# Performance work log

Measured on AMD Instinct MI355X. Metric: run time of the kernel, lower is better.

## Reference

```python
import jax, jax.numpy as jnp
import numpy as np


def pairwise_distances(x):
    # squared euclidean distances, clamped at 0 (as in the torch source)
    sq = jnp.sum(x * x, axis=1)  # [N]
    dist = sq[:, None] + sq[None, :] - 2.0 * (x @ x.T)  # [N, N]
    return jnp.maximum(dist, 0.0)


def setup_inputs() -> dict:
    key = jax.random.key(0)
    k1, k2 = jax.random.split(key)
    N, D, T = 8192, 128, 1_000_000
    features = jax.random.normal(k1, (N, D), dtype=jnp.float32)
    triplets = jax.random.randint(k2, (T, 3), 0, N, dtype=jnp.int64)
    return {"features": features, "triplets": triplets}


def reference(features, triplets):
    dist = pairwise_distances(features)  # [N, N]
    i, j, k = triplets[:, 0], triplets[:, 1], triplets[:, 2]
    d_ij = dist[i, j]  # [T] gather
    d_ik = dist[i, k]  # [T] gather
    # log(1 + exp(d_ij - d_ik)) per triplet, mean over triplets
    per_triplet = jnp.logaddexp(0.0, d_ij - d_ik)
    loss = jnp.mean(per_triplet)
    return loss.reshape(1)  # torch returns FloatTensor([loss])
```

## Files before the change

kernel.cpp:

```cpp
#include <hip/hip_runtime.h>
#include <hip/hip_fp16.h>
#include <math.h>

constexpr int D = 128;
constexpr int MAIN_BLOCKS = 2048;
constexpr int BLOCK = 256;
constexpr int NWAVES = MAIN_BLOCKS * (BLOCK / 64);
constexpr int NROWS = 8192;

#define QSCALE 25.4f
#define TWO_S2 (2.0f * (5.0f / 127.0f) * (5.0f / 127.0f))

#if __has_builtin(__builtin_amdgcn_sdot4)
__device__ inline int dot4(unsigned a, unsigned b, int c) {
    return __builtin_amdgcn_sdot4(a, b, c, false);
}
#else
__device__ inline int dot4(unsigned a, unsigned b, int c) {
    c += (int)(char)(a) * (int)(char)(b);
    c += (int)(char)(a >> 8) * (int)(char)(b >> 8);
    c += (int)(char)(a >> 16) * (int)(char)(b >> 16);
    c += (int)(char)(a >> 24) * (int)(char)(b >> 24);
    return c;
}
#endif

__global__ __launch_bounds__(256) void prep_kernel(const float* __restrict__ feat,
                                                   const unsigned long long* __restrict__ trip,
                                                   int n_slots,
                                                   __half* __restrict__ sqh,
                                                   unsigned* __restrict__ q8,
                                                   int* __restrict__ flag, int N) {
    if (blockIdx.x == gridDim.x - 1) {
        if (threadIdx.x < 64) {
            int cnt = n_slots < 2048 ? n_slots : 2048;
            bool big = false;
            for (int idx = threadIdx.x; idx < cnt; idx += 64)
                big |= (trip[idx] >> 32) != 0ULL;
            unsigned long long b = __ballot(big);
            if (threadIdx.x == 0) flag[0] = (b != 0ULL) ? 1 : 0;
        }
        return;
    }
    int gidx = blockIdx.x * 256 + threadIdx.x;
    int row = gidx >> 5, lane = gidx & 31;
    if (row >= N) return;
    float4 v = ((const float4*)(feat + (size_t)row * D))[lane];
    float s = v.x * v.x + v.y * v.y + v.z * v.z + v.w * v.w;
#pragma unroll
    for (int m = 16; m >= 1; m >>= 1) s += __shfl_xor(s, m);
    if (lane == 0) sqh[row] = __float2half(s);
    int q0 = __float2int_rn(fminf(fmaxf(v.x * QSCALE, -127.f), 127.f));
    int q1 = __float2int_rn(fminf(fmaxf(v.y * QSCALE, -127.f), 127.f));
    int q2 = __float2int_rn(fminf(fmaxf(v.z * QSCALE, -127.f), 127.f));
    int q3 = __float2int_rn(fminf(fmaxf(v.w * QSCALE, -127.f), 127.f));
    unsigned p = (q0 & 255) | ((q1 & 255) << 8) | ((q2 & 255) << 16) | ((q3 & 255) << 24);
    q8[(size_t)row * 32 + lane] = p;
}

__global__ __launch_bounds__(256, 8) void triplet_kernel(const uint4* __restrict__ q8,
                                                         const void* __restrict__ trip_raw,
                                                         const __half* __restrict__ sqh,
                                                         const int* __restrict__ flag,
                                                         double* __restrict__ partial,
                                                         int T, int N) {
    __shared__ uint4 sq_u4[NROWS * 2 / 16];
    {
        const uint4* src = (const uint4*)sqh;
        int nvec = N * 2 / 16;
        for (int t = threadIdx.x; t < nvec; t += BLOCK) sq_u4[t] = src[t];
    }
    __syncthreads();
    const __half* sqs = (const __half*)sq_u4;

    const int lane = threadIdx.x & 63;
    const int sub = lane & 3;
    const int g = lane >> 2;
    const int wave = blockIdx.x * (BLOCK / 64) + (threadIdx.x >> 6);
    const int stride = gridDim.x * (BLOCK / 64) * 16;
    const bool m32 = (flag[0] != 0);
    const int* __restrict__ t32 = (const int*)trip_raw;
    const long long* __restrict__ t64 = (const long long*)trip_raw;

    double lsum = 0.0;
    for (int tb = wave * 16; tb < T; tb += stride) {
        int t = tb + g;
        bool valid = t < T;
        int tc = valid ? t : T - 1;
        int i, j, k;
        if (m32) { i = t32[3 * tc]; j = t32[3 * tc + 1]; k = t32[3 * tc + 2]; }
        else     { i = (int)t64[3 * tc]; j = (int)t64[3 * tc + 1]; k = (int)t64[3 * tc + 2]; }

        const uint4* pi = q8 + (size_t)i * 8 + sub;
        const uint4* pj = q8 + (size_t)j * 8 + sub;
        const uint4* pk = q8 + (size_t)k * 8 + sub;
        uint4 A0 = pi[0], A1 = pi[4];
        uint4 B0 = pj[0], B1 = pj[4];
        uint4 C0 = pk[0], C1 = pk[4];

        int d1 = 0, d2 = 0;
        d1 = dot4(A0.x, B0.x, d1); d1 = dot4(A0.y, B0.y, d1);
        d1 = dot4(A0.z, B0.z, d1); d1 = dot4(A0.w, B0.w, d1);
        d1 = dot4(A1.x, B1.x, d1); d1 = dot4(A1.y, B1.y, d1);
        d1 = dot4(A1.z, B1.z, d1); d1 = dot4(A1.w, B1.w, d1);
        d2 = dot4(A0.x, C0.x, d2); d2 = dot4(A0.y, C0.y, d2);
        d2 = dot4(A0.z, C0.z, d2); d2 = dot4(A0.w, C0.w, d2);
        d2 = dot4(A1.x, C1.x, d2); d2 = dot4(A1.y, C1.y, d2);
        d2 = dot4(A1.z, C1.z, d2); d2 = dot4(A1.w, C1.w, d2);

        int dd = d1 - d2;
        dd += __shfl_xor(dd, 1);
        dd += __shfl_xor(dd, 2);

        float sqj = __half2float(sqs[j]);
        float sqk = __half2float(sqs[k]);
        float z = (sqj - sqk) - TWO_S2 * (float)dd;
        float loss = fmaxf(z, 0.0f) + __logf(1.0f + __expf(-fabsf(z)));
        lsum += valid ? (double)loss : 0.0;
    }
#pragma unroll
    for (int m = 1; m < 64; m <<= 1) lsum += __shfl_xor(lsum, m);
    if (lane == 0) partial[wave] = lsum;
}

__global__ __launch_bounds__(256) void finalize_kernel(const double* __restrict__ partial,
                                                       int nw, float* __restrict__ out,
                                                       int T) {
    __shared__ double sm[256];
    double s = 0.0;
    for (int i = threadIdx.x; i < nw; i += blockDim.x) s += partial[i];
    sm[threadIdx.x] = s;
    __syncthreads();
    for (int w = 128; w >= 1; w >>= 1) {
        if ((int)threadIdx.x < w) sm[threadIdx.x] += sm[threadIdx.x + w];
        __syncthreads();
    }
    if (threadIdx.x == 0) out[0] = (float)(sm[0] / (4.0 * (double)T));
}

extern "C" void kernel_launch(void* const* d_in, const int* in_sizes, int n_in,
                              void* d_out, int out_size, void* d_ws, size_t ws_size,
                              hipStream_t stream) {
    const float* feat = (const float*)d_in[0];
    const void* trip = d_in[1];
    int N = in_sizes[0] / D;
    int T = in_sizes[1] / 3;

    char* ws = (char*)d_ws;
    int* flag = (int*)ws;
    double* partial = (double*)(ws + 256);
    __half* sqh = (__half*)(ws + 256 + 8 * (size_t)NWAVES);
    size_t q8_off = (256 + 8 * (size_t)NWAVES + 2 * (size_t)N + 255) & ~(size_t)255;
    unsigned* q8 = (unsigned*)(ws + q8_off);
    float* out = (float*)d_out;

    int prep_blocks = (N * 32) / 256 + 1;
    prep_kernel<<<prep_blocks, 256, 0, stream>>>(feat, (const unsigned long long*)trip,
                                                 in_sizes[1], sqh, q8, flag, N);
    triplet_kernel<<<MAIN_BLOCKS, BLOCK, 0, stream>>>((const uint4*)q8, trip, sqh, flag,
                                                      partial, T, N);
    finalize_kernel<<<1, 256, 0, stream>>>(partial, NWAVES, out, T);
}
```

Before: 103.1 us.

## Process two triplet groups per iteration and prefetch next indices

Each wave now handles two 16-triplet groups per loop iteration and loads the next iteration's triplet indices before the current dot products. This raises memory-level parallelism for the random row gathers and hides index-load latency. Grid size and the occupancy hint are lowered to match the heavier per-wave work, which raises register use and may reduce the number of resident waves.

```diff
diff --git a/kernel.cpp b/kernel.cpp
--- a/kernel.cpp
+++ b/kernel.cpp
@@ -3,7 +3,7 @@
 #include <math.h>
 
 constexpr int D = 128;
-constexpr int MAIN_BLOCKS = 2048;
+constexpr int MAIN_BLOCKS = 1536;
 constexpr int BLOCK = 256;
 constexpr int NWAVES = MAIN_BLOCKS * (BLOCK / 64);
 constexpr int NROWS = 8192;
@@ -24,6 +24,15 @@
     return c;
 }
 #endif
+
+__device__ inline int dot_rows(uint4 a0, uint4 a1, uint4 b0, uint4 b1) {
+    int d = 0;
+    d = dot4(a0.x, b0.x, d); d = dot4(a0.y, b0.y, d);
+    d = dot4(a0.z, b0.z, d); d = dot4(a0.w, b0.w, d);
+    d = dot4(a1.x, b1.x, d); d = dot4(a1.y, b1.y, d);
+    d = dot4(a1.z, b1.z, d); d = dot4(a1.w, b1.w, d);
+    return d;
+}
 
 __global__ __launch_bounds__(256) void prep_kernel(const float* __restrict__ feat,
                                                    const unsigned long long* __restrict__ trip,
@@ -58,7 +67,7 @@
     q8[(size_t)row * 32 + lane] = p;
 }
 
-__global__ __launch_bounds__(256, 8) void triplet_kernel(const uint4* __restrict__ q8,
+__global__ __launch_bounds__(256, 6) void triplet_kernel(const uint4* __restrict__ q8,
                                                          const void* __restrict__ trip_raw,
                                                          const __half* __restrict__ sqh,
                                                          const int* __restrict__ flag,
@@ -77,46 +86,68 @@
     const int sub = lane & 3;
     const int g = lane >> 2;
     const int wave = blockIdx.x * (BLOCK / 64) + (threadIdx.x >> 6);
-    const int stride = gridDim.x * (BLOCK / 64) * 16;
+    const int stride = gridDim.x * (BLOCK / 64) * 32;
     const bool m32 = (flag[0] != 0);
     const int* __restrict__ t32 = (const int*)trip_raw;
     const long long* __restrict__ t64 = (const long long*)trip_raw;
 
     double lsum = 0.0;
-    for (int tb = wave * 16; tb < T; tb += stride) {
-        int t = tb + g;
-        bool valid = t < T;
-        int tc = valid ? t : T - 1;
-        int i, j, k;
-        if (m32) { i = t32[3 * tc]; j = t32[3 * tc + 1]; k = t32[3 * tc + 2]; }
-        else     { i = (int)t64[3 * tc]; j = (int)t64[3 * tc + 1]; k = (int)t64[3 * tc + 2]; }
+    int iA, jA, kA, iB, jB, kB;
+    {
+        int t0 = wave * 32;
+        int tA = (t0 + g) < T ? (t0 + g) : T - 1;
+        int tB = (t0 + 16 + g) < T ? (t0 + 16 + g) : T - 1;
+        if (m32) {
+            iA = t32[3 * tA]; jA = t32[3 * tA + 1]; kA = t32[3 * tA + 2];
+            iB = t32[3 * tB]; jB = t32[3 * tB + 1]; kB = t32[3 * tB + 2];
+        } else {
+            iA = (int)t64[3 * tA]; jA = (int)t64[3 * tA + 1]; kA = (int)t64[3 * tA + 2];
+            iB = (int)t64[3 * tB]; jB = (int)t64[3 * tB + 1]; kB = (int)t64[3 * tB + 2];
+        }
+    }
 
-        const uint4* pi = q8 + (size_t)i * 8 + sub;
-        const uint4* pj = q8 + (size_t)j * 8 + sub;
-        const uint4* pk = q8 + (size_t)k * 8 + sub;
-        uint4 A0 = pi[0], A1 = pi[4];
-        uint4 B0 = pj[0], B1 = pj[4];
-        uint4 C0 = pk[0], C1 = pk[4];
+    for (int tb = wave * 32; tb < T; tb += stride) {
+        const uint4* pAi = q8 + (size_t)iA * 8 + sub;
+        const uint4* pAj = q8 + (size_t)jA * 8 + sub;
+        const uint4* pAk = q8 + (size_t)kA * 8 + sub;
+        const uint4* pBi = q8 + (size_t)iB * 8 + sub;
+        const uint4* pBj = q8 + (size_t)jB * 8 + sub;
+        const uint4* pBk = q8 + (size_t)kB * 8 + sub;
+        uint4 Aa0 = pAi[0], Aa1 = pAi[4];
+        uint4 Ab0 = pAj[0], Ab1 = pAj[4];
+        uint4 Ac0 = pAk[0], Ac1 = pAk[4];
+        uint4 Ba0 = pBi[0], Ba1 = pBi[4];
+        uint4 Bb0 = pBj[0], Bb1 = pBj[4];
+        uint4 Bc0 = pBk[0], Bc1 = pBk[4];
 
-        int d1 = 0, d2 = 0;
-        d1 = dot4(A0.x, B0.x, d1); d1 = dot4(A0.y, B0.y, d1);
-        d1 = dot4(A0.z, B0.z, d1); d1 = dot4(A0.w, B0.w, d1);
-        d1 = dot4(A1.x, B1.x, d1); d1 = dot4(A1.y, B1.y, d1);
-        d1 = dot4(A1.z, B1.z, d1); d1 = dot4(A1.w, B1.w, d1);
-        d2 = dot4(A0.x, C0.x, d2); d2 = dot4(A0.y, C0.y, d2);
-        d2 = dot4(A0.z, C0.z, d2); d2 = dot4(A0.w, C0.w, d2);
-        d2 = dot4(A1.x, C1.x, d2); d2 = dot4(A1.y, C1.y, d2);
-        d2 = dot4(A1.z, C1.z, d2); d2 = dot4(A1.w, C1.w, d2);
+        float sqjA = __half2float(sqs[jA]);
+        float sqkA = __half2float(sqs[kA]);
+        float sqjB = __half2float(sqs[jB]);
+        float sqkB = __half2float(sqs[kB]);
+        bool vA = (tb + g) < T;
+        bool vB = (tb + 16 + g) < T;
 
-        int dd = d1 - d2;
-        dd += __shfl_xor(dd, 1);
-        dd += __shfl_xor(dd, 2);
+        int tn = tb + stride;
+        int tA = (tn + g) < T ? (tn + g) : T - 1;
+        int tB = (tn + 16 + g) < T ? (tn + 16 + g) : T - 1;
+        if (m32) {
+            iA = t32[3 * tA]; jA = t32[3 * tA + 1]; kA = t32[3 * tA + 2];
+            iB = t32[3 * tB]; jB = t32[3 * tB + 1]; kB = t32[3 * tB + 2];
+        } else {
+            iA = (int)t64[3 * tA]; jA = (int)t64[3 * tA + 1]; kA = (int)t64[3 * tA + 2];
+            iB = (int)t64[3 * tB]; jB = (int)t64[3 * tB + 1]; kB = (int)t64[3 * tB + 2];
+        }
 
-        float sqj = __half2float(sqs[j]);
-        float sqk = __half2float(sqs[k]);
-        float z = (sqj - sqk) - TWO_S2 * (float)dd;
-        float loss = fmaxf(z, 0.0f) + __logf(1.0f + __expf(-fabsf(z)));
-        lsum += valid ? (double)loss : 0.0;
+        int ddA = dot_rows(Aa0, Aa1, Ab0, Ab1) - dot_rows(Aa0, Aa1, Ac0, Ac1);
+        int ddB = dot_rows(Ba0, Ba1, Bb0, Bb1) - dot_rows(Ba0, Ba1, Bc0, Bc1);
+        ddA += __shfl_xor(ddA, 1); ddB += __shfl_xor(ddB, 1);
+        ddA += __shfl_xor(ddA, 2); ddB += __shfl_xor(ddB, 2);
+
+        float zA = (sqjA - sqkA) - TWO_S2 * (float)ddA;
+        float zB = (sqjB - sqkB) - TWO_S2 * (float)ddB;
+        float lossA = fmaxf(zA, 0.0f) + __logf(1.0f + __expf(-fabsf(zA)));
+        float lossB = fmaxf(zB, 0.0f) + __logf(1.0f + __expf(-fabsf(zB)));
+        lsum += (vA ? (double)lossA : 0.0) + (vB ? (double)lossB : 0.0);
     }
 #pragma unroll
     for (int m = 1; m < 64; m <<= 1) lsum += __shfl_xor(lsum, m);
```

After: 101.5 us. Within noise of the previous version (-1.5%).
